# Kernel tuning notes

Measured on AMD Instinct MI355X. Metric: run time of the kernel, lower is better.

## Reference

```python
import jax, jax.numpy as jnp
import numpy as np
import math

EMBED_DIM = 1024
NUM_HEADS = 16
HEAD_DIM = EMBED_DIM // NUM_HEADS
BATCH = 2
SEQ = 2048


def alibi_slopes(num_heads):
    def pow2_slopes(n):
        start = 2.0 ** (-(2.0 ** (-(math.log2(n) - 3))))
        return [start * (start ** i) for i in range(n)]
    if math.log2(num_heads).is_integer():
        s = pow2_slopes(num_heads)
    else:
        closest = 2 ** math.floor(math.log2(num_heads))
        s = pow2_slopes(closest)
        s += s[-1:] * (num_heads - closest)
    return jnp.asarray(s, dtype=jnp.float32)  # [H]


def setup_inputs() -> dict:
    key = jax.random.key(0)
    k1, k2, k3, k4, k5 = jax.random.split(key, 5)
    x = jax.random.normal(k1, (BATCH, SEQ, EMBED_DIM), dtype=jnp.float32)
    sd = 1.0 / math.sqrt(EMBED_DIM)
    Wqkv = jax.random.uniform(k2, (EMBED_DIM, 3 * EMBED_DIM), minval=-sd, maxval=sd, dtype=jnp.float32)
    bqkv = jax.random.uniform(k3, (3 * EMBED_DIM,), minval=-sd, maxval=sd, dtype=jnp.float32)
    Wout = jax.random.uniform(k4, (EMBED_DIM, EMBED_DIM), minval=-sd, maxval=sd, dtype=jnp.float32)
    bout = jax.random.uniform(k5, (EMBED_DIM,), minval=-sd, maxval=sd, dtype=jnp.float32)
    return {"x": x, "Wqkv": Wqkv, "bqkv": bqkv, "Wout": Wout, "bout": bout}


def reference(x, Wqkv, bqkv, Wout, bout):
    B, S, E = x.shape
    H, D = NUM_HEADS, HEAD_DIM
    qkv = x @ Wqkv + bqkv                       # [B,S,3E]
    qkv = qkv.reshape(B, S, H, 3 * D)
    q, k, v = jnp.split(qkv, 3, axis=-1)        # each [B,S,H,D]
    scores = jnp.einsum('bqhd,bkhd->bhqk', q, k) / math.sqrt(D)
    # ALiBi bias: distance[i,j] = j - i, scaled per-head
    pos = jnp.arange(S)
    distance = (pos[None, :] - pos[:, None]).astype(jnp.float32)  # [S,S]
    scores = scores + alibi_slopes(H)[None, :, None, None] * distance[None, None, :, :]
    attn = jax.nn.softmax(scores, axis=-1)      # [B,H,S,S]
    out = jnp.einsum('bhqk,bkhd->bqhd', attn, v).reshape(B, S, E)
    out = out @ Wout + bout
    return out, attn
```

## Files before the change

kernel.cpp:

```cpp
#include <hip/hip_runtime.h>

#define BATCH 2
#define SEQ   2048
#define EMB   1024
#define NH    16
#define HD    64

typedef __attribute__((ext_vector_type(8))) _Float16 half8;
typedef __attribute__((ext_vector_type(4))) _Float16 half4;
typedef __attribute__((ext_vector_type(4))) float floatx4;

#define LOG2E 1.44269504088896f

#if __has_builtin(__builtin_amdgcn_exp2f)
__device__ __forceinline__ float fexp2(float x) { return __builtin_amdgcn_exp2f(x); }
#else
__device__ __forceinline__ float fexp2(float x) { return exp2f(x); }
#endif

__global__ __launch_bounds__(256)
void cvt_f16(const float* __restrict__ in, _Float16* __restrict__ out, int n8) {
    int i = blockIdx.x * 256 + threadIdx.x;
    if (i >= n8) return;
    float4 a = ((const float4*)in)[2 * i];
    float4 b = ((const float4*)in)[2 * i + 1];
    half8 h = {(_Float16)a.x, (_Float16)a.y, (_Float16)a.z, (_Float16)a.w,
               (_Float16)b.x, (_Float16)b.y, (_Float16)b.z, (_Float16)b.w};
    ((half8*)out)[i] = h;
}

__global__ __launch_bounds__(256)
void transpose_f16(const float* __restrict__ W, _Float16* __restrict__ o,
                   int K, int N) {
    __shared__ float t[32][33];
    const int n0 = blockIdx.x * 32, k0 = blockIdx.y * 32;
    const int r = threadIdx.x >> 3, c4 = (threadIdx.x & 7) * 4;
    float4 v = *(const float4*)&W[(size_t)(k0 + r) * N + n0 + c4];
    t[r][c4 + 0] = v.x; t[r][c4 + 1] = v.y;
    t[r][c4 + 2] = v.z; t[r][c4 + 3] = v.w;
    __syncthreads();
    half4 hv;
#pragma unroll
    for (int j = 0; j < 4; ++j) hv[j] = (_Float16)t[c4 + j][r];
    *(half4*)&o[(size_t)(n0 + r) * K + k0 + c4] = hv;
}

#define ALD 40

__global__ __launch_bounds__(256)
void gemm_qkv_mfma(const _Float16* __restrict__ Xh, const _Float16* __restrict__ Wh,
                   const float* __restrict__ bias,
                   _Float16* __restrict__ Qh, _Float16* __restrict__ Kh,
                   _Float16* __restrict__ Vh) {
    const int K = EMB;
    __shared__ _Float16 Ah[128 * ALD];
    __shared__ _Float16 Bh[128 * ALD];

    const int tid  = threadIdx.x;
    const int wave = tid >> 6, lane = tid & 63;
    const int quad = lane >> 4, lp = lane & 15;

    const int linear = blockIdx.y * 24 + blockIdx.x;
    const int swz = (linear & 7) * 96 + (linear >> 3);
    const int bx = swz % 24, by = swz / 24;
    const int row0 = by * 128, col0 = bx * 128;
    const int wm = (wave >> 1) * 64, wn = (wave & 1) * 64;

    const int srow = tid >> 2, sseg = (tid & 3) * 8;

    floatx4 acc[4][4];
#pragma unroll
    for (int i = 0; i < 4; ++i)
#pragma unroll
        for (int j = 0; j < 4; ++j) acc[i][j] = (floatx4){0.f, 0.f, 0.f, 0.f};

    for (int k0 = 0; k0 < K; k0 += 32) {
#pragma unroll
        for (int it = 0; it < 2; ++it) {
            int r = srow + it * 64;
            *(uint4*)&Ah[r * ALD + sseg] =
                *(const uint4*)&Xh[(size_t)(row0 + r) * K + k0 + sseg];
            *(uint4*)&Bh[r * ALD + sseg] =
                *(const uint4*)&Wh[(size_t)(col0 + r) * K + k0 + sseg];
        }
        __syncthreads();

        half8 ah[4];
#pragma unroll
        for (int mi = 0; mi < 4; ++mi)
            ah[mi] = *(const half8*)&Ah[(wm + mi * 16 + lp) * ALD + quad * 8];
#pragma unroll
        for (int ni = 0; ni < 4; ++ni) {
            half8 bh = *(const half8*)&Bh[(wn + ni * 16 + lp) * ALD + quad * 8];
#pragma unroll
            for (int mi = 0; mi < 4; ++mi)
                acc[mi][ni] = __builtin_amdgcn_mfma_f32_16x16x32_f16(
                    ah[mi], bh, acc[mi][ni], 0, 0, 0);
        }
        __syncthreads();
    }

#pragma unroll
    for (int ni = 0; ni < 4; ++ni) {
        const int c = col0 + wn + ni * 16 + lp;
        const int h = c / 192;
        const int rem = c - h * 192;
        const int which = rem >> 6;
        const int d = rem & 63;
        _Float16* __restrict__ P = (which == 0) ? Qh : (which == 1) ? Kh : Vh;
        const float bb = bias[c];
#pragma unroll
        for (int mi = 0; mi < 4; ++mi) {
            floatx4 a = acc[mi][ni];
#pragma unroll
            for (int r = 0; r < 4; ++r) {
                int m = row0 + wm + mi * 16 + quad * 4 + r;
                int b = m >> 11, s = m & (SEQ - 1);
                P[((size_t)(b * NH + h) * SEQ + s) * HD + d] =
                    (_Float16)(a[r] + bb);
            }
        }
    }
}

__global__ __launch_bounds__(256)
void gemm_out_mfma(const _Float16* __restrict__ Ch, const _Float16* __restrict__ Oh,
                   const float* __restrict__ bias, float* __restrict__ out) {
    const int K = EMB, N = EMB;
    __shared__ _Float16 Ah[128 * ALD];
    __shared__ _Float16 Bh[128 * ALD];

    const int tid  = threadIdx.x;
    const int wave = tid >> 6, lane = tid & 63;
    const int quad = lane >> 4, lp = lane & 15;

    const int linear = blockIdx.y * 8 + blockIdx.x;
    const int swz = (linear & 7) * 32 + (linear >> 3);
    const int bx = swz & 7, by = swz >> 3;
    const int row0 = by * 128, col0 = bx * 128;
    const int wm = (wave >> 1) * 64, wn = (wave & 1) * 64;

    const int srow = tid >> 2, sseg = (tid & 3) * 8;

    floatx4 acc[4][4];
#pragma unroll
    for (int i = 0; i < 4; ++i)
#pragma unroll
        for (int j = 0; j < 4; ++j) acc[i][j] = (floatx4){0.f, 0.f, 0.f, 0.f};

    for (int k0 = 0; k0 < K; k0 += 32) {
#pragma unroll
        for (int it = 0; it < 2; ++it) {
            int r = srow + it * 64;
            *(uint4*)&Ah[r * ALD + sseg] =
                *(const uint4*)&Ch[(size_t)(row0 + r) * K + k0 + sseg];
            *(uint4*)&Bh[r * ALD + sseg] =
                *(const uint4*)&Oh[(size_t)(col0 + r) * K + k0 + sseg];
        }
        __syncthreads();

        half8 ah[4];
#pragma unroll
        for (int mi = 0; mi < 4; ++mi)
            ah[mi] = *(const half8*)&Ah[(wm + mi * 16 + lp) * ALD + quad * 8];
#pragma unroll
        for (int ni = 0; ni < 4; ++ni) {
            half8 bh = *(const half8*)&Bh[(wn + ni * 16 + lp) * ALD + quad * 8];
#pragma unroll
            for (int mi = 0; mi < 4; ++mi)
                acc[mi][ni] = __builtin_amdgcn_mfma_f32_16x16x32_f16(
                    ah[mi], bh, acc[mi][ni], 0, 0, 0);
        }
        __syncthreads();
    }

#pragma unroll
    for (int ni = 0; ni < 4; ++ni) {
        const int c = col0 + wn + ni * 16 + lp;
        const float bb = bias[c];
#pragma unroll
        for (int mi = 0; mi < 4; ++mi) {
            floatx4 a = acc[mi][ni];
#pragma unroll
            for (int r = 0; r < 4; ++r) {
                int m = row0 + wm + mi * 16 + quad * 4 + r;
                out[(size_t)m * N + c] = a[r] + bb;
            }
        }
    }
}

#define QT 128
#define KT 64
#define LDST 72
#define NTILE (SEQ / KT)

__global__ __launch_bounds__(512)
void attn_mfma(const _Float16* __restrict__ Qh,
               const _Float16* __restrict__ Kh,
               const _Float16* __restrict__ Vh,
               float* __restrict__ attn,
               _Float16* __restrict__ ctx) {
    __shared__ _Float16 qs[QT * LDST];
    __shared__ _Float16 ksb[2][KT * LDST];
    __shared__ _Float16 vtb[2][HD * LDST];
    __shared__ _Float16 ps[QT * LDST];

    const int tid  = threadIdx.x;
    const int wave = tid >> 6, lane = tid & 63;
    const int quad = lane >> 4, lp = lane & 15;
    const int q0 = blockIdx.x * QT;
    const int bh = blockIdx.y;
    const int h  = bh & (NH - 1);
    const float slope2 = exp2f(-0.5f * (float)(h + 1)) * LOG2E;
    const float scale2 = 0.125f * LOG2E;
    const float step   = slope2 * (float)KT;

    const _Float16* Qbase = Qh + ((size_t)bh * SEQ + q0) * HD;
    const _Float16* Kbase = Kh + (size_t)bh * SEQ * HD;
    const _Float16* Vbase = Vh + (size_t)bh * SEQ * HD;

    const int srow = tid >> 3, sseg = tid & 7;
    const int kbase = srow ^ (sseg << 3);

    for (int c = tid; c < QT * HD / 8; c += 512) {
        int row = c >> 3, seg = c & 7;
        *(uint4*)&qs[row * LDST + seg * 8] =
            *(const uint4*)&Qbase[(size_t)row * HD + seg * 8];
    }
    uint4 kreg = *(const uint4*)&Kbase[(size_t)srow * HD + sseg * 8];
    *(uint4*)&ksb[0][srow * LDST + sseg * 8] = kreg;
    __syncthreads();

    const half8 qa0 = *(const half8*)&qs[(16 * wave + lp) * LDST + quad * 8];
    const half8 qa1 = *(const half8*)&qs[(16 * wave + lp) * LDST + 32 + quad * 8];

    const int qg = q0 + 16 * wave + lp;

    float m0 = -1e30f, mxv = -1e30f, lsum = 0.f;

    float ali[4][4];
#pragma unroll
    for (int t = 0; t < 4; ++t)
#pragma unroll
        for (int r = 0; r < 4; ++r)
            ali[t][r] = slope2 * (float)(16 * t + 4 * quad + r - qg);

    int cur = 0;
    for (int kt = 0; kt < NTILE; ++kt) {
        if (kt) __syncthreads();
        if (kt + 1 < NTILE)
            kreg = *(const uint4*)&Kbase[(size_t)(kt + 1) * KT * HD +
                                         (size_t)srow * HD + sseg * 8];
        const _Float16* ks = ksb[cur];

        floatx4 cc[4];
#pragma unroll
        for (int t = 0; t < 4; ++t) {
            half8 b0 = *(const half8*)&ks[(16 * t + lp) * LDST + quad * 8];
            half8 b1 = *(const half8*)&ks[(16 * t + lp) * LDST + 32 + quad * 8];
            floatx4 c = {0.f, 0.f, 0.f, 0.f};
            c = __builtin_amdgcn_mfma_f32_16x16x32_f16(b0, qa0, c, 0, 0, 0);
            cc[t] = __builtin_amdgcn_mfma_f32_16x16x32_f16(b1, qa1, c, 0, 0, 0);
        }
        float sv[4][4];
        float tm = -1e30f;
#pragma unroll
        for (int t = 0; t < 4; ++t)
#pragma unroll
            for (int r = 0; r < 4; ++r) {
                float s = fmaf(cc[t][r], scale2, ali[t][r]);
                sv[t][r] = s;
                tm = fmaxf(tm, s);
            }
        mxv = fmaxf(mxv, tm);
        if (mxv > m0 + 8.f) {
            lsum *= fexp2(m0 - mxv);
            m0 = mxv;
        }
#pragma unroll
        for (int t = 0; t < 4; ++t)
#pragma unroll
            for (int r = 0; r < 4; ++r) lsum += fexp2(sv[t][r] - m0);
#pragma unroll
        for (int t = 0; t < 4; ++t)
#pragma unroll
            for (int r = 0; r < 4; ++r) ali[t][r] += step;

        if (kt + 1 < NTILE) {
            *(uint4*)&ksb[cur ^ 1][srow * LDST + sseg * 8] = kreg;
            cur ^= 1;
        }
    }

    float off2;
    {
        float mm = mxv;
        float ll = lsum * fexp2(m0 - mm);
#pragma unroll
        for (int off = 16; off < 64; off <<= 1) {
            float mo = __shfl_xor(mm, off);
            float lo = __shfl_xor(ll, off);
            float mn = fmaxf(mm, mo);
            ll = ll * fexp2(mm - mn) + lo * fexp2(mo - mn);
            mm = mn;
        }
        off2 = mm + __log2f(ll);
    }

    floatx4 o[4];
#pragma unroll
    for (int t = 0; t < 4; ++t) o[t] = (floatx4){0.f, 0.f, 0.f, 0.f};

    float* arow = attn + (size_t)bh * SEQ * SEQ +
                  (size_t)(q0 + 16 * wave + lp) * SEQ + 4 * quad;

    float ali2[4][4];
#pragma unroll
    for (int t = 0; t < 4; ++t)
#pragma unroll
        for (int r = 0; r < 4; ++r)
            ali2[t][r] = slope2 * (float)(16 * t + 4 * quad + r - qg) - off2;

    __syncthreads();
    uint4 vreg;
    kreg = *(const uint4*)&Kbase[(size_t)srow * HD + sseg * 8];
    vreg = *(const uint4*)&Vbase[(size_t)srow * HD + sseg * 8];
    *(uint4*)&ksb[0][srow * LDST + sseg * 8] = kreg;
    {
        union { uint4 u; _Float16 e[8]; } vv; vv.u = vreg;
#pragma unroll
        for (int j = 0; j < 8; ++j)
            vtb[0][(sseg * 8 + j) * LDST + kbase] = vv.e[j];
    }
    __syncthreads();

    cur = 0;
    for (int kt = 0; kt < NTILE; ++kt) {
        if (kt) __syncthreads();
        if (kt + 1 < NTILE) {
            size_t goff = (size_t)(kt + 1) * KT * HD + (size_t)srow * HD + sseg * 8;
            kreg = *(const uint4*)&Kbase[goff];
            vreg = *(const uint4*)&Vbase[goff];
        }
        const _Float16* ks = ksb[cur];
        const _Float16* vt = vtb[cur];

#pragma unroll
        for (int t = 0; t < 4; ++t) {
            half8 b0 = *(const half8*)&ks[(16 * t + lp) * LDST + quad * 8];
            half8 b1 = *(const half8*)&ks[(16 * t + lp) * LDST + 32 + quad * 8];
            floatx4 c = {0.f, 0.f, 0.f, 0.f};
            c = __builtin_amdgcn_mfma_f32_16x16x32_f16(b0, qa0, c, 0, 0, 0);
            c = __builtin_amdgcn_mfma_f32_16x16x32_f16(b1, qa1, c, 0, 0, 0);
            float p0 = fexp2(fmaf(c[0], scale2, ali2[t][0]));
            float p1 = fexp2(fmaf(c[1], scale2, ali2[t][1]));
            float p2 = fexp2(fmaf(c[2], scale2, ali2[t][2]));
            float p3 = fexp2(fmaf(c[3], scale2, ali2[t][3]));
            float4 pw = {p0, p1, p2, p3};
            *(float4*)&arow[kt * KT + 16 * t] = pw;
            const int col = 16 * t + 4 * quad;
            half4 ph = {(_Float16)p0, (_Float16)p1, (_Float16)p2, (_Float16)p3};
            *(half4*)&ps[(16 * wave + lp) * LDST + col] = ph;
        }

        half8 pa0 = *(const half8*)&ps[(16 * wave + lp) * LDST + quad * 8];
        half8 pa1 = *(const half8*)&ps[(16 * wave + lp) * LDST + 32 + quad * 8];
#pragma unroll
        for (int t = 0; t < 4; ++t) {
            int g = 2 * t + (lp >> 3);
            half8 vb0 = *(const half8*)&vt[(16 * t + lp) * LDST + ((quad ^ g) << 3)];
            half8 vb1 = *(const half8*)&vt[(16 * t + lp) * LDST + (((quad + 4) ^ g) << 3)];
            o[t] = __builtin_amdgcn_mfma_f32_16x16x32_f16(pa0, vb0, o[t], 0, 0, 0);
            o[t] = __builtin_amdgcn_mfma_f32_16x16x32_f16(pa1, vb1, o[t], 0, 0, 0);
        }

#pragma unroll
        for (int t = 0; t < 4; ++t)
#pragma unroll
            for (int r = 0; r < 4; ++r) ali2[t][r] += step;

        if (kt + 1 < NTILE) {
            *(uint4*)&ksb[cur ^ 1][srow * LDST + sseg * 8] = kreg;
            union { uint4 u; _Float16 e[8]; } vv; vv.u = vreg;
#pragma unroll
            for (int j = 0; j < 8; ++j)
                vtb[cur ^ 1][(sseg * 8 + j) * LDST + kbase] = vv.e[j];
            cur ^= 1;
        }
    }

    const int b = bh >> 4;
#pragma unroll
    for (int t = 0; t < 4; ++t)
#pragma unroll
        for (int r = 0; r < 4; ++r)
            ctx[((size_t)(b * SEQ + q0 + 16 * wave + quad * 4 + r)) * EMB +
                h * HD + 16 * t + lp] = (_Float16)o[t][r];
}


extern "C" void kernel_launch(void* const* d_in, const int* in_sizes, int n_in,
                              void* d_out, int out_size, void* d_ws, size_t ws_size,
                              hipStream_t stream) {
    const float* x    = (const float*)d_in[0];
    const float* Wqkv = (const float*)d_in[1];
    const float* bqkv = (const float*)d_in[2];
    const float* Wout = (const float*)d_in[3];
    const float* bout = (const float*)d_in[4];

    float* out  = (float*)d_out;
    float* attn = out + (size_t)BATCH * SEQ * EMB;

    const size_t HE = (size_t)BATCH * NH * SEQ * HD;
    const size_t XE = (size_t)BATCH * SEQ * EMB;
    _Float16* Qh = (_Float16*)d_ws;
    _Float16* Kh = Qh + HE;
    _Float16* Vh = Kh + HE;
    _Float16* Ch = Vh + HE;
    _Float16* Xh = Ch + XE;
    _Float16* Wh = Xh + XE;
    _Float16* Oh = Wh + (size_t)3 * EMB * EMB;

    cvt_f16<<<dim3(2048), dim3(256), 0, stream>>>(x, Xh, (int)(XE / 8));
    transpose_f16<<<dim3(96, 32), dim3(256), 0, stream>>>(Wqkv, Wh, EMB, 3 * EMB);
    transpose_f16<<<dim3(32, 32), dim3(256), 0, stream>>>(Wout, Oh, EMB, EMB);

    gemm_qkv_mfma<<<dim3(24, 32), dim3(256), 0, stream>>>(
        Xh, Wh, bqkv, Qh, Kh, Vh);

    attn_mfma<<<dim3(SEQ / QT, BATCH * NH), dim3(512), 0, stream>>>(
        Qh, Kh, Vh, attn, Ch);

    gemm_out_mfma<<<dim3(8, 32), dim3(256), 0, stream>>>(Ch, Oh, bout, out);
}
```

Before: 270.8 us.

## Load Q and K fragments directly from global memory, dropping K shared staging

```diff
diff --git a/kernel.cpp b/kernel.cpp
--- a/kernel.cpp
+++ b/kernel.cpp
@@ -195,14 +195,12 @@
 #define LDST 72
 #define NTILE (SEQ / KT)
 
-__global__ __launch_bounds__(512)
+__global__ __launch_bounds__(512, 6)
 void attn_mfma(const _Float16* __restrict__ Qh,
                const _Float16* __restrict__ Kh,
                const _Float16* __restrict__ Vh,
                float* __restrict__ attn,
                _Float16* __restrict__ ctx) {
-    __shared__ _Float16 qs[QT * LDST];
-    __shared__ _Float16 ksb[2][KT * LDST];
     __shared__ _Float16 vtb[2][HD * LDST];
     __shared__ _Float16 ps[QT * LDST];
 
@@ -214,83 +212,44 @@
     const int h  = bh & (NH - 1);
     const float slope2 = exp2f(-0.5f * (float)(h + 1)) * LOG2E;
     const float scale2 = 0.125f * LOG2E;
-    const float step   = slope2 * (float)KT;
 
     const _Float16* Qbase = Qh + ((size_t)bh * SEQ + q0) * HD;
     const _Float16* Kbase = Kh + (size_t)bh * SEQ * HD;
     const _Float16* Vbase = Vh + (size_t)bh * SEQ * HD;
 
-    const int srow = tid >> 3, sseg = tid & 7;
-    const int kbase = srow ^ (sseg << 3);
-
-    for (int c = tid; c < QT * HD / 8; c += 512) {
-        int row = c >> 3, seg = c & 7;
-        *(uint4*)&qs[row * LDST + seg * 8] =
-            *(const uint4*)&Qbase[(size_t)row * HD + seg * 8];
-    }
-    uint4 kreg = *(const uint4*)&Kbase[(size_t)srow * HD + sseg * 8];
-    *(uint4*)&ksb[0][srow * LDST + sseg * 8] = kreg;
-    __syncthreads();
-
-    const half8 qa0 = *(const half8*)&qs[(16 * wave + lp) * LDST + quad * 8];
-    const half8 qa1 = *(const half8*)&qs[(16 * wave + lp) * LDST + 32 + quad * 8];
+    const half8 qa0 = *(const half8*)&Qbase[(size_t)(16 * wave + lp) * HD + quad * 8];
+    const half8 qa1 = *(const half8*)&Qbase[(size_t)(16 * wave + lp) * HD + 32 + quad * 8];
 
     const int qg = q0 + 16 * wave + lp;
+    const float aq = -slope2 * (float)qg;
 
     float m0 = -1e30f, mxv = -1e30f, lsum = 0.f;
 
-    float ali[4][4];
-#pragma unroll
-    for (int t = 0; t < 4; ++t)
-#pragma unroll
-        for (int r = 0; r < 4; ++r)
-            ali[t][r] = slope2 * (float)(16 * t + 4 * quad + r - qg);
-
-    int cur = 0;
     for (int kt = 0; kt < NTILE; ++kt) {
-        if (kt) __syncthreads();
-        if (kt + 1 < NTILE)
-            kreg = *(const uint4*)&Kbase[(size_t)(kt + 1) * KT * HD +
-                                         (size_t)srow * HD + sseg * 8];
-        const _Float16* ks = ksb[cur];
-
-        floatx4 cc[4];
+        const _Float16* Kt = Kbase + (size_t)kt * KT * HD;
+        __builtin_amdgcn_s_setprio(1);
 #pragma unroll
         for (int t = 0; t < 4; ++t) {
-            half8 b0 = *(const half8*)&ks[(16 * t + lp) * LDST + quad * 8];
-            half8 b1 = *(const half8*)&ks[(16 * t + lp) * LDST + 32 + quad * 8];
+            half8 b0 = *(const half8*)&Kt[(size_t)(16 * t + lp) * HD + quad * 8];
+            half8 b1 = *(const half8*)&Kt[(size_t)(16 * t + lp) * HD + 32 + quad * 8];
             floatx4 c = {0.f, 0.f, 0.f, 0.f};
             c = __builtin_amdgcn_mfma_f32_16x16x32_f16(b0, qa0, c, 0, 0, 0);
-            cc[t] = __builtin_amdgcn_mfma_f32_16x16x32_f16(b1, qa1, c, 0, 0, 0);
-        }
-        float sv[4][4];
-        float tm = -1e30f;
-#pragma unroll
-        for (int t = 0; t < 4; ++t)
-#pragma unroll
-            for (int r = 0; r < 4; ++r) {
-                float s = fmaf(cc[t][r], scale2, ali[t][r]);
-                sv[t][r] = s;
-                tm = fmaxf(tm, s);
+            c = __builtin_amdgcn_mfma_f32_16x16x32_f16(b1, qa1, c, 0, 0, 0);
+            float kb = (float)(kt * KT + 16 * t + 4 * quad);
+            float s0 = fmaf(c[0], scale2, fmaf(slope2, kb,       aq));
+            float s1 = fmaf(c[1], scale2, fmaf(slope2, kb + 1.f, aq));
+            float s2 = fmaf(c[2], scale2, fmaf(slope2, kb + 2.f, aq));
+            float s3 = fmaf(c[3], scale2, fmaf(slope2, kb + 3.f, aq));
+            float tm = fmaxf(fmaxf(s0, s1), fmaxf(s2, s3));
+            mxv = fmaxf(mxv, tm);
+            if (mxv > m0 + 8.f) {
+                lsum *= fexp2(m0 - mxv);
+                m0 = mxv;
             }
-        mxv = fmaxf(mxv, tm);
-        if (mxv > m0 + 8.f) {
-            lsum *= fexp2(m0 - mxv);
-            m0 = mxv;
-        }
-#pragma unroll
-        for (int t = 0; t < 4; ++t)
-#pragma unroll
-            for (int r = 0; r < 4; ++r) lsum += fexp2(sv[t][r] - m0);
-#pragma unroll
-        for (int t = 0; t < 4; ++t)
-#pragma unroll
-            for (int r = 0; r < 4; ++r) ali[t][r] += step;
-
-        if (kt + 1 < NTILE) {
-            *(uint4*)&ksb[cur ^ 1][srow * LDST + sseg * 8] = kreg;
-            cur ^= 1;
-        }
+            lsum += fexp2(s0 - m0) + fexp2(s1 - m0) +
+                    fexp2(s2 - m0) + fexp2(s3 - m0);
+        }
+        __builtin_amdgcn_s_setprio(0);
     }
 
     float off2;
@@ -314,58 +273,53 @@
 
     float* arow = attn + (size_t)bh * SEQ * SEQ +
                   (size_t)(q0 + 16 * wave + lp) * SEQ + 4 * quad;
-
-    float ali2[4][4];
-#pragma unroll
-    for (int t = 0; t < 4; ++t)
-#pragma unroll
-        for (int r = 0; r < 4; ++r)
-            ali2[t][r] = slope2 * (float)(16 * t + 4 * quad + r - qg) - off2;
-
-    __syncthreads();
-    uint4 vreg;
-    kreg = *(const uint4*)&Kbase[(size_t)srow * HD + sseg * 8];
-    vreg = *(const uint4*)&Vbase[(size_t)srow * HD + sseg * 8];
-    *(uint4*)&ksb[0][srow * LDST + sseg * 8] = kreg;
+    const float aq2 = aq - off2;
+
+    const int srow = tid >> 3, sseg = tid & 7;
+    const int kvx = srow ^ (sseg << 3);
+
+    uint4 vreg = *(const uint4*)&Vbase[(size_t)srow * HD + sseg * 8];
     {
         union { uint4 u; _Float16 e[8]; } vv; vv.u = vreg;
 #pragma unroll
         for (int j = 0; j < 8; ++j)
-            vtb[0][(sseg * 8 + j) * LDST + kbase] = vv.e[j];
+            vtb[0][(sseg * 8 + j) * LDST + kvx] = vv.e[j];
     }
     __syncthreads();
 
-    cur = 0;
+    int cur = 0;
     for (int kt = 0; kt < NTILE; ++kt) {
         if (kt) __syncthreads();
-        if (kt + 1 < NTILE) {
-            size_t goff = (size_t)(kt + 1) * KT * HD + (size_t)srow * HD + sseg * 8;
-            kreg = *(const uint4*)&Kbase[goff];
-            vreg = *(const uint4*)&Vbase[goff];
-        }
-        const _Float16* ks = ksb[cur];
+        if (kt + 1 < NTILE)
+            vreg = *(const uint4*)&Vbase[(size_t)(kt + 1) * KT * HD +
+                                         (size_t)srow * HD + sseg * 8];
+        const _Float16* Kt = Kbase + (size_t)kt * KT * HD;
         const _Float16* vt = vtb[cur];
 
+        __builtin_amdgcn_s_setprio(1);
 #pragma unroll
         for (int t = 0; t < 4; ++t) {
-            half8 b0 = *(const half8*)&ks[(16 * t + lp) * LDST + quad * 8];
-            half8 b1 = *(const half8*)&ks[(16 * t + lp) * LDST + 32 + quad * 8];
+            half8 b0 = *(const half8*)&Kt[(size_t)(16 * t + lp) * HD + quad * 8];
+            half8 b1 = *(const half8*)&Kt[(size_t)(16 * t + lp) * HD + 32 + quad * 8];
             floatx4 c = {0.f, 0.f, 0.f, 0.f};
             c = __builtin_amdgcn_mfma_f32_16x16x32_f16(b0, qa0, c, 0, 0, 0);
             c = __builtin_amdgcn_mfma_f32_16x16x32_f16(b1, qa1, c, 0, 0, 0);
-            float p0 = fexp2(fmaf(c[0], scale2, ali2[t][0]));
-            float p1 = fexp2(fmaf(c[1], scale2, ali2[t][1]));
-            float p2 = fexp2(fmaf(c[2], scale2, ali2[t][2]));
-            float p3 = fexp2(fmaf(c[3], scale2, ali2[t][3]));
+            float kb = (float)(kt * KT + 16 * t + 4 * quad);
+            float p0 = fexp2(fmaf(c[0], scale2, fmaf(slope2, kb,       aq2)));
+            float p1 = fexp2(fmaf(c[1], scale2, fmaf(slope2, kb + 1.f, aq2)));
+            float p2 = fexp2(fmaf(c[2], scale2, fmaf(slope2, kb + 2.f, aq2)));
+            float p3 = fexp2(fmaf(c[3], scale2, fmaf(slope2, kb + 3.f, aq2)));
             float4 pw = {p0, p1, p2, p3};
             *(float4*)&arow[kt * KT + 16 * t] = pw;
             const int col = 16 * t + 4 * quad;
             half4 ph = {(_Float16)p0, (_Float16)p1, (_Float16)p2, (_Float16)p3};
             *(half4*)&ps[(16 * wave + lp) * LDST + col] = ph;
         }
+        __builtin_amdgcn_s_setprio(0);
 
         half8 pa0 = *(const half8*)&ps[(16 * wave + lp) * LDST + quad * 8];
         half8 pa1 = *(const half8*)&ps[(16 * wave + lp) * LDST + 32 + quad * 8];
+        __builtin_amdgcn_s_setprio(1);
 #pragma unroll
         for (int t = 0; t < 4; ++t) {
             int g = 2 * t + (lp >> 3);
@@ -374,18 +328,13 @@
             o[t] = __builtin_amdgcn_mfma_f32_16x16x32_f16(pa0, vb0, o[t], 0, 0, 0);
             o[t] = __builtin_amdgcn_mfma_f32_16x16x32_f16(pa1, vb1, o[t], 0, 0, 0);
         }
-
-#pragma unroll
-        for (int t = 0; t < 4; ++t)
-#pragma unroll
-            for (int r = 0; r < 4; ++r) ali2[t][r] += step;
+        __builtin_amdgcn_s_setprio(0);
 
         if (kt + 1 < NTILE) {
-            *(uint4*)&ksb[cur ^ 1][srow * LDST + sseg * 8] = kreg;
             union { uint4 u; _Float16 e[8]; } vv; vv.u = vreg;
 #pragma unroll
             for (int j = 0; j < 8; ++j)
-                vtb[cur ^ 1][(sseg * 8 + j) * LDST + kbase] = vv.e[j];
+                vtb[cur ^ 1][(sseg * 8 + j) * LDST + kvx] = vv.e[j];
             cur ^= 1;
         }
     }
```

After: 459.5 us. +69.7%, slower.
